# Kernel optimization log

Measured on AMD Instinct MI355X. Metric: run time of the kernel, lower is better.

## Reference

```python
import jax, jax.numpy as jnp
import numpy as np

N = 100000; E = 1600000; G = 512; L = 1000
FXD = 4; FXT = 5; H = 64; NOUT = 2

def setup_inputs() -> dict:
    key = jax.random.key(0)
    ks = jax.random.split(key, 16)
    x = jax.random.normal(ks[0], (N, FXD), dtype=jnp.float32)
    edge_index = jax.random.randint(ks[1], (2, E), 0, N, dtype=jnp.int64)
    # contiguous, non-empty graph assignment (sorted)
    batch = jnp.minimum(jnp.arange(N, dtype=jnp.int64) // (N // G), G - 1)
    target = jax.random.normal(ks[2], (G, L, FXT), dtype=jnp.float32)
    def lin(k, fi, fo):
        s = 1.0 / np.sqrt(fi)
        k1, k2 = jax.random.split(k)
        return (jax.random.uniform(k1, (fi, fo), jnp.float32, -s, s),
                jax.random.uniform(k2, (fo,), jnp.float32, -s, s))
    W1, b1 = lin(ks[3], FXD, H)
    W2, b2 = lin(ks[4], H, 2 * H)
    Wg, bg = lin(ks[5], 2 * H, H)
    s = 1.0 / np.sqrt(FXT * 3)
    Wc = jax.random.uniform(ks[6], (H, FXT, 3), jnp.float32, -s, s)  # OIH
    bc = jax.random.uniform(ks[7], (H,), jnp.float32, -s, s)
    Wt, bt = lin(ks[8], H, H)
    Wf, bf = lin(ks[9], 2 * H, H)
    Wo, bo = lin(ks[10], H, NOUT)
    return dict(x=x, edge_index=edge_index, batch=batch, target=target,
                W1=W1, b1=b1, W2=W2, b2=b2, Wg=Wg, bg=bg,
                Wc=Wc, bc=bc, Wt=Wt, bt=bt, Wf=Wf, bf=bf, Wo=Wo, bo=bo)

def _gcn_prep(edge_index):
    # add self-loops, compute symmetric normalization (PyG gcn_norm)
    loops = jnp.arange(N, dtype=edge_index.dtype)
    row = jnp.concatenate([edge_index[0], loops])
    col = jnp.concatenate([edge_index[1], loops])
    deg = jax.ops.segment_sum(jnp.ones_like(col, dtype=jnp.float32), col, num_segments=N)
    dis = jnp.where(deg > 0, jax.lax.rsqrt(deg), 0.0)
    norm = dis[row] * dis[col]  # [E+N]
    return row, col, norm

def _gcn_conv(h, row, col, norm):
    # gather-scale-scatter aggregation
    msg = h[row] * norm[:, None]
    return jax.ops.segment_sum(msg, col, num_segments=N)

def reference(x, edge_index, batch, target, W1, b1, W2, b2, Wg, bg, Wc, bc, Wt, bt, Wf, bf, Wo, bo):
    row, col, norm = _gcn_prep(edge_index)
    h = jax.nn.relu(_gcn_conv(x @ W1, row, col, norm) + b1)
    h = jax.nn.relu(_gcn_conv(h @ W2, row, col, norm) + b2)
    g = jax.ops.segment_max(h, batch, num_segments=G)  # global_max_pool [G, 2H]
    g = g @ Wg + bg  # dropout = identity (eval)
    t = jnp.transpose(target, (0, 2, 1))  # [G, FXT, L]
    t = jax.lax.conv_general_dilated(t, Wc, (1,), 'VALID',
                                     dimension_numbers=('NCH', 'OIH', 'NCH')) + bc[None, :, None]
    t = jax.nn.relu(t)
    t = jnp.max(t, axis=-1)  # AdaptiveMaxPool1d(1) [G, H]
    t = t @ Wt + bt
    xc = jnp.concatenate([g, t], axis=1)
    xc = jax.nn.relu(xc @ Wf + bf)
    return xc @ Wo + bo
```

## Files before the change

### kernel.cpp

```cpp
#include <hip/hip_runtime.h>
#include <hip/hip_bf16.h>

constexpr int N   = 100000;
constexpr int E   = 1600000;
constexpr int G   = 512;
constexpr int L   = 1000;
constexpr int NPG = 195;

constexpr int SLOTS = 48;
constexpr int NR2   = 256;
constexpr int RS2   = 391;
constexpr int PCAP2 = 6912;
constexpr int BCH   = 4096;

typedef __attribute__((ext_vector_type(8))) short bf16x8;
typedef __attribute__((ext_vector_type(4))) float f32x4;

__device__ __forceinline__ float bf2f(__hip_bfloat16 b) { return __bfloat162float(b); }
__device__ __forceinline__ float lo_bf(unsigned v) { return __uint_as_float(v << 16); }
__device__ __forceinline__ float hi_bf(unsigned v) { return __uint_as_float(v & 0xFFFF0000u); }
__device__ __forceinline__ unsigned packbf2(float a, float b) {
    __hip_bfloat16 ha = __float2bfloat16(a), hb = __float2bfloat16(b);
    unsigned short ua = *(unsigned short*)&ha, ub = *(unsigned short*)&hb;
    return (unsigned)ua | ((unsigned)ub << 16);
}


__global__ void k_init(int* __restrict__ pcnt, const float* __restrict__ W2,
                       short* __restrict__ W2hi, short* __restrict__ W2lo) {
    int i = blockIdx.x * 256 + threadIdx.x;
    if (i < NR2) pcnt[i] = 0;
    if (i < 64 * 128) {
        float w = W2[i];
        __hip_bfloat16 h = __float2bfloat16(w);
        float r = w - __bfloat162float(h);
        __hip_bfloat16 l = __float2bfloat16(r);
        W2hi[i] = *(short*)&h;
        W2lo[i] = *(short*)&l;
    }
}


__global__ void __launch_bounds__(256) k_part(
        const int* __restrict__ row, const int* __restrict__ col,
        int* __restrict__ pcnt, unsigned* __restrict__ precs) {
    __shared__ unsigned rec_s[BCH];
    __shared__ unsigned char rr_s[BCH];
    __shared__ int cnt_s[NR2], base_s[NR2], cur_s[NR2];
    int tid = threadIdx.x;
    cnt_s[tid] = 0;
    __syncthreads();
    int e0 = blockIdx.x * BCH;
    int nE = min(BCH, E - e0);
    for (int i = tid; i < nE; i += 256) {
        int c = __builtin_nontemporal_load(col + e0 + i);
        int r = __builtin_nontemporal_load(row + e0 + i);
        int rr = c / RS2;
        rec_s[i] = ((unsigned)r << 9) | (unsigned)(c - rr * RS2);
        rr_s[i] = (unsigned char)rr;
        atomicAdd(&cnt_s[rr], 1);
    }
    __syncthreads();
    base_s[tid] = atomicAdd(&pcnt[tid], cnt_s[tid]);
    cur_s[tid] = 0;
    __syncthreads();
    for (int i = tid; i < nE; i += 256) {
        int rr = rr_s[i];
        int p = base_s[rr] + atomicAdd(&cur_s[rr], 1);
        if (p < PCAP2) precs[rr * PCAP2 + p] = rec_s[i];
    }
}


__global__ void __launch_bounds__(256) k_sort(
        const int* __restrict__ pcnt, const unsigned* __restrict__ precs,
        int* __restrict__ slots, int* __restrict__ cursor, float* __restrict__ dis) {
    __shared__ unsigned recs[PCAP2];
    __shared__ int hist[512], off[512], off2[512], ps[256];
    int tid = threadIdx.x;
    int rr = blockIdx.x;
    int cnt = min(pcnt[rr], PCAP2);
    hist[tid] = 0; hist[tid + 256] = 0;
    __syncthreads();
    const unsigned* pr = precs + rr * PCAP2;
    for (int i = tid; i < cnt; i += 256) {
        unsigned r = pr[i];
        recs[i] = r;
        atomicAdd(&hist[r & 511], 1);
    }
    __syncthreads();
    int h0 = hist[2 * tid], h1 = hist[2 * tid + 1];
    int s = h0 + h1;
    ps[tid] = s;
    __syncthreads();
    for (int d = 1; d < 256; d <<= 1) {
        int v = (tid >= d) ? ps[tid - d] : 0;
        __syncthreads();
        ps[tid] += v;
        __syncthreads();
    }
    int excl = ps[tid] - s;
    off[2 * tid] = excl;       off[2 * tid + 1] = excl + h0;
    off2[2 * tid] = excl;      off2[2 * tid + 1] = excl + h0;
    __syncthreads();
    for (int ln = tid; ln < RS2; ln += 256) {
        int n = rr * RS2 + ln;
        if (n < N) {
            int c = hist[ln];
            dis[n] = rsqrtf((float)c + 1.0f);
            cursor[n] = n * SLOTS + min(c, SLOTS);
        }
    }
    for (int i = tid; i < cnt; i += 256) {
        unsigned r = recs[i];
        int ln = (int)(r & 511u);
        int p = atomicAdd(&off2[ln], 1);
        int j = p - off[ln];
        if (j < SLOTS) slots[(rr * RS2 + ln) * SLOTS + j] = (int)(r >> 9);
    }
}


__global__ void __launch_bounds__(256) k_gather_x(
        const int* __restrict__ cursor, const int* __restrict__ slots,
        const float* __restrict__ dis, const float4* __restrict__ x,
        float4* __restrict__ aggx) {
    int n = blockIdx.x * 256 + threadIdx.x;
    if (n >= N) return;
    int s = n * SLOTS;
    int cnt = cursor[n] - s;
    float dn = dis[n];
    float4 a = make_float4(0.f, 0.f, 0.f, 0.f);
    int j = 0;
    for (; j + 4 <= cnt; j += 4) {
        int s0 = slots[s + j], s1 = slots[s + j + 1],
            s2 = slots[s + j + 2], s3 = slots[s + j + 3];
        float w0 = dis[s0], w1 = dis[s1], w2 = dis[s2], w3 = dis[s3];
        float4 v0 = x[s0], v1 = x[s1], v2 = x[s2], v3 = x[s3];
        a.x = fmaf(v0.x, w0, a.x); a.y = fmaf(v0.y, w0, a.y);
        a.z = fmaf(v0.z, w0, a.z); a.w = fmaf(v0.w, w0, a.w);
        a.x = fmaf(v1.x, w1, a.x); a.y = fmaf(v1.y, w1, a.y);
        a.z = fmaf(v1.z, w1, a.z); a.w = fmaf(v1.w, w1, a.w);
        a.x = fmaf(v2.x, w2, a.x); a.y = fmaf(v2.y, w2, a.y);
        a.z = fmaf(v2.z, w2, a.z); a.w = fmaf(v2.w, w2, a.w);
        a.x = fmaf(v3.x, w3, a.x); a.y = fmaf(v3.y, w3, a.y);
        a.z = fmaf(v3.z, w3, a.z); a.w = fmaf(v3.w, w3, a.w);
    }
    for (; j < cnt; j++) {
        int sx = slots[s + j];
        float w = dis[sx];
        float4 v = x[sx];
        a.x = fmaf(v.x, w, a.x); a.y = fmaf(v.y, w, a.y);
        a.z = fmaf(v.z, w, a.z); a.w = fmaf(v.w, w, a.w);
    }
    float4 xs = x[n];
    float sl = dn * dn;
    a.x = fmaf(xs.x, sl, a.x * dn);
    a.y = fmaf(xs.y, sl, a.y * dn);
    a.z = fmaf(xs.z, sl, a.z * dn);
    a.w = fmaf(xs.w, sl, a.w * dn);
    aggx[n] = a;
}

__global__ void __launch_bounds__(256) k_layer1(
        const float4* __restrict__ aggx,
        const float* __restrict__ W1, const float* __restrict__ b1,
        __hip_bfloat16* __restrict__ h) {
    __shared__ float w1s[256];
    __shared__ float b1s[64];
    int tid = threadIdx.x;
    w1s[tid] = W1[tid];
    if (tid < 64) b1s[tid] = b1[tid];
    __syncthreads();
    int idx = blockIdx.x * 256 + tid;
    int n = idx >> 6;
    int f = idx & 63;
    if (n >= N) return;
    float4 a = aggx[n];
    float v = b1s[f];
    v = fmaf(a.x, w1s[f], v);
    v = fmaf(a.y, w1s[64 + f], v);
    v = fmaf(a.z, w1s[128 + f], v);
    v = fmaf(a.w, w1s[192 + f], v);
    h[idx] = __float2bfloat16(fmaxf(v, 0.0f));
}


__global__ void __launch_bounds__(256) k_gather_h(
        const int* __restrict__ cursor, const int* __restrict__ slots,
        const float* __restrict__ dis, const unsigned* __restrict__ h32,
        unsigned* __restrict__ aggh32) {
    __shared__ int   ls[8][SLOTS];
    __shared__ float lw[8][SLOTS];
    __shared__ int   lcnt[8];
    int tid = threadIdx.x;
    int nb = blockIdx.x * 8;
    if (tid < 8) {
        int node = nb + tid;
        lcnt[tid] = (node < N) ? (cursor[node] - node * SLOTS) : 0;
    }
    __syncthreads();
    for (int i = tid; i < 8 * SLOTS; i += 256) {
        int lo = i / SLOTS, j = i % SLOTS;
        if (j < lcnt[lo]) {
            int src = slots[(nb + lo) * SLOTS + j];
            ls[lo][j] = src;
            lw[lo][j] = dis[src];
        }
    }
    __syncthreads();
    int wid = tid >> 6, lane = tid & 63;
    int half = lane >> 5, li = lane & 31;
    int local = wid * 2 + half;
    int n = nb + local;
    if (n >= N) return;
    int cnt = lcnt[local];
    float dn = dis[n];
    float acc0 = 0.0f, acc1 = 0.0f;
    int j = 0;
    for (; j + 8 <= cnt; j += 8) {
        unsigned v[8]; float w[8];
        #pragma unroll
        for (int k = 0; k < 8; k++) {
            int src = ls[local][j + k];
            v[k] = h32[(size_t)src * 32 + li];
            w[k] = lw[local][j + k];
        }
        #pragma unroll
        for (int k = 0; k < 8; k++) {
            acc0 = fmaf(w[k], lo_bf(v[k]), acc0);
            acc1 = fmaf(w[k], hi_bf(v[k]), acc1);
        }
    }
    for (; j < cnt; j++) {
        int src = ls[local][j];
        unsigned v = h32[(size_t)src * 32 + li];
        float w = lw[local][j];
        acc0 = fmaf(w, lo_bf(v), acc0);
        acc1 = fmaf(w, hi_bf(v), acc1);
    }
    unsigned sv = h32[(size_t)n * 32 + li];
    acc0 = fmaf(dn, lo_bf(sv), acc0) * dn;
    acc1 = fmaf(dn, hi_bf(sv), acc1) * dn;
    aggh32[(size_t)n * 32 + li] = packbf2(acc0, acc1);
}


__global__ void __launch_bounds__(256) k_mfma_pool(
        const __hip_bfloat16* __restrict__ aggh,
        const short* __restrict__ W2hi, const short* __restrict__ W2lo,
        const float* __restrict__ b2, float* __restrict__ gbuf) {
    int tid = threadIdx.x;
    int wid = tid >> 6, lane = tid & 63;
    int m = lane & 15, quad = lane >> 4;
    int gi = blockIdx.x;
    int n0 = gi * NPG;
    int n1 = (gi == G - 1) ? N : n0 + NPG;
    int cb0 = wid * 32, cb1 = cb0 + 16;
    bf16x8 bh[2][2], bl[2][2];
    #pragma unroll
    for (int t = 0; t < 2; t++) {
        int cb = cb0 + t * 16;
        #pragma unroll
        for (int ks = 0; ks < 2; ks++) {
            bf16x8 hh, ll;
            #pragma unroll
            for (int j = 0; j < 8; j++) {
                int k = ks * 32 + quad * 8 + j;
                hh[j] = W2hi[k * 128 + cb + m];
                ll[j] = W2lo[k * 128 + cb + m];
            }
            bh[t][ks] = hh; bl[t][ks] = ll;
        }
    }
    float bias0 = b2[cb0 + m], bias1 = b2[cb1 + m];
    const short* ah = (const short*)aggh;
    float mx0 = 0.0f, mx1 = 0.0f;
    bf16x8 a0, a1;
    {
        const short* p = ah + (size_t)(n0 + m) * 64 + quad * 8;
        a0 = *(const bf16x8*)p;
        a1 = *(const bf16x8*)(p + 32);
    }
    for (int bn = n0; bn < n1; bn += 16) {
        bf16x8 na0 = a0, na1 = a1;
        if (bn + 16 < n1) {
            const short* p = ah + (size_t)(bn + 16 + m) * 64 + quad * 8;
            na0 = *(const bf16x8*)p;
            na1 = *(const bf16x8*)(p + 32);
        }
        f32x4 acc0 = {0.f, 0.f, 0.f, 0.f};
        f32x4 acc1 = {0.f, 0.f, 0.f, 0.f};
        acc0 = __builtin_amdgcn_mfma_f32_16x16x32_bf16(a0, bh[0][0], acc0, 0, 0, 0);
        acc0 = __builtin_amdgcn_mfma_f32_16x16x32_bf16(a1, bh[0][1], acc0, 0, 0, 0);
        acc0 = __builtin_amdgcn_mfma_f32_16x16x32_bf16(a0, bl[0][0], acc0, 0, 0, 0);
        acc0 = __builtin_amdgcn_mfma_f32_16x16x32_bf16(a1, bl[0][1], acc0, 0, 0, 0);
        acc1 = __builtin_amdgcn_mfma_f32_16x16x32_bf16(a0, bh[1][0], acc1, 0, 0, 0);
        acc1 = __builtin_amdgcn_mfma_f32_16x16x32_bf16(a1, bh[1][1], acc1, 0, 0, 0);
        acc1 = __builtin_amdgcn_mfma_f32_16x16x32_bf16(a0, bl[1][0], acc1, 0, 0, 0);
        acc1 = __builtin_amdgcn_mfma_f32_16x16x32_bf16(a1, bl[1][1], acc1, 0, 0, 0);
        int rb = bn + quad * 4;
        #pragma unroll
        for (int r = 0; r < 4; r++) {
            float v0 = fmaxf(acc0[r] + bias0, 0.0f);
            float v1 = fmaxf(acc1[r] + bias1, 0.0f);
            if (rb + r < n1) {
                mx0 = fmaxf(mx0, v0);
                mx1 = fmaxf(mx1, v1);
            }
        }
        a0 = na0; a1 = na1;
    }
    mx0 = fmaxf(mx0, __shfl_xor(mx0, 16));
    mx0 = fmaxf(mx0, __shfl_xor(mx0, 32));
    mx1 = fmaxf(mx1, __shfl_xor(mx1, 16));
    mx1 = fmaxf(mx1, __shfl_xor(mx1, 32));
    if (quad == 0) {
        gbuf[gi * 128 + cb0 + m] = mx0;
        gbuf[gi * 128 + cb1 + m] = mx1;
    }
}


__global__ void __launch_bounds__(256) k_conv(
        const float* __restrict__ target, const float* __restrict__ Wc,
        const float* __restrict__ bc, float* __restrict__ tb) {
    __shared__ float tg[L * 5];
    __shared__ float pm[4 * 64];
    int tid = threadIdx.x;
    int gi = blockIdx.x;
    const float* tsrc = target + (size_t)gi * (L * 5);
    for (int i = tid; i < L * 5; i += 256) tg[i] = tsrc[i];
    __syncthreads();
    int co = tid & 63, rr = tid >> 6;
    float wc[15];
    #pragma unroll
    for (int j = 0; j < 15; j++) wc[j] = Wc[co * 15 + j];
    int p0 = rr * 250;
    int pend = min(p0 + 250, 998);
    float a0 = tg[p0 * 5 + 0], a1 = tg[p0 * 5 + 1], a2 = tg[p0 * 5 + 2],
          a3 = tg[p0 * 5 + 3], a4 = tg[p0 * 5 + 4];
    float b0 = tg[p0 * 5 + 5], b1 = tg[p0 * 5 + 6], b2 = tg[p0 * 5 + 7],
          b3 = tg[p0 * 5 + 8], b4 = tg[p0 * 5 + 9];
    float m = -1e30f;
    for (int p = p0; p < pend; p++) {
        const float* cp = &tg[(p + 2) * 5];
        float c0 = cp[0], c1 = cp[1], c2 = cp[2], c3 = cp[3], c4 = cp[4];
        float v = 0.0f;
        v = fmaf(a0, wc[0],  v); v = fmaf(b0, wc[1],  v); v = fmaf(c0, wc[2],  v);
        v = fmaf(a1, wc[3],  v); v = fmaf(b1, wc[4],  v); v = fmaf(c1, wc[5],  v);
        v = fmaf(a2, wc[6],  v); v = fmaf(b2, wc[7],  v); v = fmaf(c2, wc[8],  v);
        v = fmaf(a3, wc[9],  v); v = fmaf(b3, wc[10], v); v = fmaf(c3, wc[11], v);
        v = fmaf(a4, wc[12], v); v = fmaf(b4, wc[13], v); v = fmaf(c4, wc[14], v);
        m = fmaxf(m, v);
        a0 = b0; a1 = b1; a2 = b2; a3 = b3; a4 = b4;
        b0 = c0; b1 = c1; b2 = c2; b3 = c3; b4 = c4;
    }
    pm[rr * 64 + co] = m;
    __syncthreads();
    if (tid < 64) {
        float mm = fmaxf(fmaxf(pm[tid], pm[64 + tid]), fmaxf(pm[128 + tid], pm[192 + tid]));
        tb[gi * 64 + tid] = fmaxf(mm + bc[tid], 0.0f);
    }
}


__global__ void __launch_bounds__(64) k_head(
        const float* __restrict__ gbuf, const float* __restrict__ tb,
        const float* __restrict__ Wg, const float* __restrict__ bg,
        const float* __restrict__ Wt, const float* __restrict__ bt,
        const float* __restrict__ Wf, const float* __restrict__ bf,
        const float* __restrict__ Wo, const float* __restrict__ bo,
        float* __restrict__ out) {
    __shared__ float grs[128], ts[64], g2s[64], t2s[64], xcs[64];
    int tid = threadIdx.x;
    int gi = blockIdx.x;
    grs[tid]      = gbuf[gi * 128 + tid];
    grs[64 + tid] = gbuf[gi * 128 + 64 + tid];
    ts[tid]       = tb[gi * 64 + tid];
    __syncthreads();
    float a = bg[tid];
    #pragma unroll 8
    for (int k = 0; k < 128; k++) a = fmaf(grs[k], Wg[k * 64 + tid], a);
    float b = bt[tid];
    #pragma unroll 8
    for (int k = 0; k < 64; k++) b = fmaf(ts[k], Wt[k * 64 + tid], b);
    g2s[tid] = a;
    t2s[tid] = b;
    __syncthreads();
    float c = bf[tid];
    #pragma unroll 8
    for (int k = 0; k < 64; k++) c = fmaf(g2s[k], Wf[k * 64 + tid], c);
    #pragma unroll 8
    for (int k = 0; k < 64; k++) c = fmaf(t2s[k], Wf[(64 + k) * 64 + tid], c);
    c = fmaxf(c, 0.0f);
    xcs[tid] = c;
    __syncthreads();
    if (tid < 2) {
        float o = bo[tid];
        for (int k = 0; k < 64; k++) o = fmaf(xcs[k], Wo[k * 2 + tid], o);
        out[gi * 2 + tid] = o;
    }
}


extern "C" void kernel_launch(void* const* d_in, const int* in_sizes, int n_in,
                              void* d_out, int out_size, void* d_ws, size_t ws_size,
                              hipStream_t stream) {
    const float* x      = (const float*)d_in[0];
    const int*   ei     = (const int*)d_in[1];
    const float* target = (const float*)d_in[3];
    const float* W1 = (const float*)d_in[4];
    const float* b1 = (const float*)d_in[5];
    const float* W2 = (const float*)d_in[6];
    const float* b2 = (const float*)d_in[7];
    const float* Wg = (const float*)d_in[8];
    const float* bg = (const float*)d_in[9];
    const float* Wc = (const float*)d_in[10];
    const float* bc = (const float*)d_in[11];
    const float* Wt = (const float*)d_in[12];
    const float* bt = (const float*)d_in[13];
    const float* Wf = (const float*)d_in[14];
    const float* bf = (const float*)d_in[15];
    const float* Wo = (const float*)d_in[16];
    const float* bo = (const float*)d_in[17];
    float* out = (float*)d_out;

    const int* row = ei;
    const int* col = ei + E;

    char* base = (char*)d_ws;
    size_t o = 0;
    auto alloc = [&](size_t bytes) -> void* {
        void* p = base + o;
        o = (o + bytes + 255) & ~(size_t)255;
        return p;
    };
    int*      cursor = (int*)     alloc((size_t)N * 4);
    float*    dis    = (float*)   alloc((size_t)N * 4);
    int*      slots  = (int*)     alloc((size_t)N * SLOTS * 4);
    int*      pcnt   = (int*)     alloc(NR2 * 4);
    unsigned* precs  = (unsigned*)alloc((size_t)NR2 * PCAP2 * 4);
    float*    aggx   = (float*)   alloc((size_t)N * 4 * 4);
    __hip_bfloat16* h    = (__hip_bfloat16*)alloc((size_t)N * 64 * 2);
    __hip_bfloat16* aggh = (__hip_bfloat16*)alloc((size_t)N * 64 * 2);
    short*    W2hi   = (short*)   alloc((size_t)64 * 128 * 2);
    short*    W2lo   = (short*)   alloc((size_t)64 * 128 * 2);
    float*    gbuf   = (float*)   alloc((size_t)G * 128 * 4);
    float*    tb     = (float*)   alloc((size_t)G * 64 * 4);

    k_init     <<<32, 256, 0, stream>>>(pcnt, W2, W2hi, W2lo);
    k_part     <<<(E + BCH - 1) / BCH, 256, 0, stream>>>(row, col, pcnt, precs);
    k_sort     <<<NR2, 256, 0, stream>>>(pcnt, precs, slots, cursor, dis);
    k_gather_x <<<(N + 255) / 256, 256, 0, stream>>>(cursor, slots, dis,
                                                     (const float4*)x, (float4*)aggx);
    k_layer1   <<<(N * 64 + 255) / 256, 256, 0, stream>>>((const float4*)aggx, W1, b1, h);
    k_gather_h <<<(N + 7) / 8, 256, 0, stream>>>(cursor, slots, dis,
                                                 (const unsigned*)h, (unsigned*)aggh);
    k_mfma_pool<<<G, 256, 0, stream>>>(aggh, W2hi, W2lo, b2, gbuf);
    k_conv     <<<G, 256, 0, stream>>>(target, Wc, bc, tb);
    k_head     <<<G, 64, 0, stream>>>(gbuf, tb, Wg, bg, Wt, bt, Wf, bf, Wo, bo, out);
}
```

Measured before the change: 278.0 us.

## Fuse layer-1 gather with linear layer and fold head MLP into pool kernel

Merges the x-aggregation gather and the layer-1 linear+ReLU into one kernel, staging aggregated features in shared memory and writing packed bf16 pairs. This removes the aggx intermediate buffer and one launch. It also moves the head MLP into the tail of the MFMA pooling kernel, run by the first wavefront after a block sync, which drops gbuf and the separate head launch. The cost is that the head now runs serially in one wave per block, and conv must finish before pooling.

```diff
diff --git a/kernel.cpp b/kernel.cpp
--- a/kernel.cpp
+++ b/kernel.cpp
@@ -121,68 +121,75 @@
 }
 
 
-__global__ void __launch_bounds__(256) k_gather_x(
+__global__ void __launch_bounds__(256) k_gxl1(
         const int* __restrict__ cursor, const int* __restrict__ slots,
         const float* __restrict__ dis, const float4* __restrict__ x,
-        float4* __restrict__ aggx) {
-    int n = blockIdx.x * 256 + threadIdx.x;
-    if (n >= N) return;
-    int s = n * SLOTS;
-    int cnt = cursor[n] - s;
-    float dn = dis[n];
-    float4 a = make_float4(0.f, 0.f, 0.f, 0.f);
-    int j = 0;
-    for (; j + 4 <= cnt; j += 4) {
-        int s0 = slots[s + j], s1 = slots[s + j + 1],
-            s2 = slots[s + j + 2], s3 = slots[s + j + 3];
-        float w0 = dis[s0], w1 = dis[s1], w2 = dis[s2], w3 = dis[s3];
-        float4 v0 = x[s0], v1 = x[s1], v2 = x[s2], v3 = x[s3];
-        a.x = fmaf(v0.x, w0, a.x); a.y = fmaf(v0.y, w0, a.y);
-        a.z = fmaf(v0.z, w0, a.z); a.w = fmaf(v0.w, w0, a.w);
-        a.x = fmaf(v1.x, w1, a.x); a.y = fmaf(v1.y, w1, a.y);
-        a.z = fmaf(v1.z, w1, a.z); a.w = fmaf(v1.w, w1, a.w);
-        a.x = fmaf(v2.x, w2, a.x); a.y = fmaf(v2.y, w2, a.y);
-        a.z = fmaf(v2.z, w2, a.z); a.w = fmaf(v2.w, w2, a.w);
-        a.x = fmaf(v3.x, w3, a.x); a.y = fmaf(v3.y, w3, a.y);
-        a.z = fmaf(v3.z, w3, a.z); a.w = fmaf(v3.w, w3, a.w);
-    }
-    for (; j < cnt; j++) {
-        int sx = slots[s + j];
-        float w = dis[sx];
-        float4 v = x[sx];
-        a.x = fmaf(v.x, w, a.x); a.y = fmaf(v.y, w, a.y);
-        a.z = fmaf(v.z, w, a.z); a.w = fmaf(v.w, w, a.w);
-    }
-    float4 xs = x[n];
-    float sl = dn * dn;
-    a.x = fmaf(xs.x, sl, a.x * dn);
-    a.y = fmaf(xs.y, sl, a.y * dn);
-    a.z = fmaf(xs.z, sl, a.z * dn);
-    a.w = fmaf(xs.w, sl, a.w * dn);
-    aggx[n] = a;
-}
-
-__global__ void __launch_bounds__(256) k_layer1(
-        const float4* __restrict__ aggx,
         const float* __restrict__ W1, const float* __restrict__ b1,
-        __hip_bfloat16* __restrict__ h) {
+        unsigned* __restrict__ h32) {
+    __shared__ float ax[256][4];
     __shared__ float w1s[256];
     __shared__ float b1s[64];
     int tid = threadIdx.x;
     w1s[tid] = W1[tid];
     if (tid < 64) b1s[tid] = b1[tid];
-    __syncthreads();
-    int idx = blockIdx.x * 256 + tid;
-    int n = idx >> 6;
-    int f = idx & 63;
-    if (n >= N) return;
-    float4 a = aggx[n];
-    float v = b1s[f];
-    v = fmaf(a.x, w1s[f], v);
-    v = fmaf(a.y, w1s[64 + f], v);
-    v = fmaf(a.z, w1s[128 + f], v);
-    v = fmaf(a.w, w1s[192 + f], v);
-    h[idx] = __float2bfloat16(fmaxf(v, 0.0f));
+    int nb = blockIdx.x * 256;
+    int n = nb + tid;
+    float4 a = make_float4(0.f, 0.f, 0.f, 0.f);
+    if (n < N) {
+        int s = n * SLOTS;
+        int cnt = cursor[n] - s;
+        float dn = dis[n];
+        int j = 0;
+        for (; j + 4 <= cnt; j += 4) {
+            int s0 = slots[s + j], s1 = slots[s + j + 1],
+                s2 = slots[s + j + 2], s3 = slots[s + j + 3];
+            float w0 = dis[s0], w1 = dis[s1], w2 = dis[s2], w3 = dis[s3];
+            float4 v0 = x[s0], v1 = x[s1], v2 = x[s2], v3 = x[s3];
+            a.x = fmaf(v0.x, w0, a.x); a.y = fmaf(v0.y, w0, a.y);
+            a.z = fmaf(v0.z, w0, a.z); a.w = fmaf(v0.w, w0, a.w);
+            a.x = fmaf(v1.x, w1, a.x); a.y = fmaf(v1.y, w1, a.y);
+            a.z = fmaf(v1.z, w1, a.z); a.w = fmaf(v1.w, w1, a.w);
+            a.x = fmaf(v2.x, w2, a.x); a.y = fmaf(v2.y, w2, a.y);
+            a.z = fmaf(v2.z, w2, a.z); a.w = fmaf(v2.w, w2, a.w);
+            a.x = fmaf(v3.x, w3, a.x); a.y = fmaf(v3.y, w3, a.y);
+            a.z = fmaf(v3.z, w3, a.z); a.w = fmaf(v3.w, w3, a.w);
+        }
+        for (; j < cnt; j++) {
+            int sx = slots[s + j];
+            float w = dis[sx];
+            float4 v = x[sx];
+            a.x = fmaf(v.x, w, a.x); a.y = fmaf(v.y, w, a.y);
+            a.z = fmaf(v.z, w, a.z); a.w = fmaf(v.w, w, a.w);
+        }
+        float4 xs = x[n];
+        float sl = dn * dn;
+        a.x = fmaf(xs.x, sl, a.x * dn);
+        a.y = fmaf(xs.y, sl, a.y * dn);
+        a.z = fmaf(xs.z, sl, a.z * dn);
+        a.w = fmaf(xs.w, sl, a.w * dn);
+    }
+    ax[tid][0] = a.x; ax[tid][1] = a.y; ax[tid][2] = a.z; ax[tid][3] = a.w;
+    __syncthreads();
+    int p = tid & 31, r0 = tid >> 5;
+    int f0 = 2 * p, f1 = 2 * p + 1;
+    float wA0 = w1s[f0],       wB0 = w1s[f1];
+    float wA1 = w1s[64 + f0],  wB1 = w1s[64 + f1];
+    float wA2 = w1s[128 + f0], wB2 = w1s[128 + f1];
+    float wA3 = w1s[192 + f0], wB3 = w1s[192 + f1];
+    float bb0 = b1s[f0], bb1 = b1s[f1];
+    #pragma unroll 4
+    for (int i = 0; i < 32; i++) {
+        int ln = r0 + 8 * i;
+        int node = nb + ln;
+        if (node >= N) break;
+        float v0 = bb0, v1 = bb1;
+        float g0 = ax[ln][0], g1 = ax[ln][1], g2 = ax[ln][2], g3 = ax[ln][3];
+        v0 = fmaf(g0, wA0, v0); v1 = fmaf(g0, wB0, v1);
+        v0 = fmaf(g1, wA1, v0); v1 = fmaf(g1, wB1, v1);
+        v0 = fmaf(g2, wA2, v0); v1 = fmaf(g2, wB2, v1);
+        v0 = fmaf(g3, wA3, v0); v1 = fmaf(g3, wB3, v1);
+        h32[(size_t)node * 32 + p] = packbf2(fmaxf(v0, 0.0f), fmaxf(v1, 0.0f));
+    }
 }
 
 
@@ -243,82 +250,6 @@
     acc0 = fmaf(dn, lo_bf(sv), acc0) * dn;
     acc1 = fmaf(dn, hi_bf(sv), acc1) * dn;
     aggh32[(size_t)n * 32 + li] = packbf2(acc0, acc1);
-}
-
-
-__global__ void __launch_bounds__(256) k_mfma_pool(
-        const __hip_bfloat16* __restrict__ aggh,
-        const short* __restrict__ W2hi, const short* __restrict__ W2lo,
-        const float* __restrict__ b2, float* __restrict__ gbuf) {
-    int tid = threadIdx.x;
-    int wid = tid >> 6, lane = tid & 63;
-    int m = lane & 15, quad = lane >> 4;
-    int gi = blockIdx.x;
-    int n0 = gi * NPG;
-    int n1 = (gi == G - 1) ? N : n0 + NPG;
-    int cb0 = wid * 32, cb1 = cb0 + 16;
-    bf16x8 bh[2][2], bl[2][2];
-    #pragma unroll
-    for (int t = 0; t < 2; t++) {
-        int cb = cb0 + t * 16;
-        #pragma unroll
-        for (int ks = 0; ks < 2; ks++) {
-            bf16x8 hh, ll;
-            #pragma unroll
-            for (int j = 0; j < 8; j++) {
-                int k = ks * 32 + quad * 8 + j;
-                hh[j] = W2hi[k * 128 + cb + m];
-                ll[j] = W2lo[k * 128 + cb + m];
-            }
-            bh[t][ks] = hh; bl[t][ks] = ll;
-        }
-    }
-    float bias0 = b2[cb0 + m], bias1 = b2[cb1 + m];
-    const short* ah = (const short*)aggh;
-    float mx0 = 0.0f, mx1 = 0.0f;
-    bf16x8 a0, a1;
-    {
-        const short* p = ah + (size_t)(n0 + m) * 64 + quad * 8;
-        a0 = *(const bf16x8*)p;
-        a1 = *(const bf16x8*)(p + 32);
-    }
-    for (int bn = n0; bn < n1; bn += 16) {
-        bf16x8 na0 = a0, na1 = a1;
-        if (bn + 16 < n1) {
-            const short* p = ah + (size_t)(bn + 16 + m) * 64 + quad * 8;
-            na0 = *(const bf16x8*)p;
-            na1 = *(const bf16x8*)(p + 32);
-        }
-        f32x4 acc0 = {0.f, 0.f, 0.f, 0.f};
-        f32x4 acc1 = {0.f, 0.f, 0.f, 0.f};
-        acc0 = __builtin_amdgcn_mfma_f32_16x16x32_bf16(a0, bh[0][0], acc0, 0, 0, 0);
-        acc0 = __builtin_amdgcn_mfma_f32_16x16x32_bf16(a1, bh[0][1], acc0, 0, 0, 0);
-        acc0 = __builtin_amdgcn_mfma_f32_16x16x32_bf16(a0, bl[0][0], acc0, 0, 0, 0);
-        acc0 = __builtin_amdgcn_mfma_f32_16x16x32_bf16(a1, bl[0][1], acc0, 0, 0, 0);
-        acc1 = __builtin_amdgcn_mfma_f32_16x16x32_bf16(a0, bh[1][0], acc1, 0, 0, 0);
-        acc1 = __builtin_amdgcn_mfma_f32_16x16x32_bf16(a1, bh[1][1], acc1, 0, 0, 0);
-        acc1 = __builtin_amdgcn_mfma_f32_16x16x32_bf16(a0, bl[1][0], acc1, 0, 0, 0);
-        acc1 = __builtin_amdgcn_mfma_f32_16x16x32_bf16(a1, bl[1][1], acc1, 0, 0, 0);
-        int rb = bn + quad * 4;
-        #pragma unroll
-        for (int r = 0; r < 4; r++) {
-            float v0 = fmaxf(acc0[r] + bias0, 0.0f);
-            float v1 = fmaxf(acc1[r] + bias1, 0.0f);
-            if (rb + r < n1) {
-                mx0 = fmaxf(mx0, v0);
-                mx1 = fmaxf(mx1, v1);
-            }
-        }
-        a0 = na0; a1 = na1;
-    }
-    mx0 = fmaxf(mx0, __shfl_xor(mx0, 16));
-    mx0 = fmaxf(mx0, __shfl_xor(mx0, 32));
-    mx1 = fmaxf(mx1, __shfl_xor(mx1, 16));
-    mx1 = fmaxf(mx1, __shfl_xor(mx1, 32));
-    if (quad == 0) {
-        gbuf[gi * 128 + cb0 + m] = mx0;
-        gbuf[gi * 128 + cb1 + m] = mx1;
-    }
 }
 
 
@@ -365,41 +296,107 @@
 }
 
 
-__global__ void __launch_bounds__(64) k_head(
-        const float* __restrict__ gbuf, const float* __restrict__ tb,
+__global__ void __launch_bounds__(256) k_mfma_pool(
+        const __hip_bfloat16* __restrict__ aggh,
+        const short* __restrict__ W2hi, const short* __restrict__ W2lo,
+        const float* __restrict__ b2, const float* __restrict__ tb,
         const float* __restrict__ Wg, const float* __restrict__ bg,
         const float* __restrict__ Wt, const float* __restrict__ bt,
         const float* __restrict__ Wf, const float* __restrict__ bf,
         const float* __restrict__ Wo, const float* __restrict__ bo,
         float* __restrict__ out) {
-    __shared__ float grs[128], ts[64], g2s[64], t2s[64], xcs[64];
-    int tid = threadIdx.x;
+    __shared__ float gvec[128], ts[64], g2s[64], t2s[64], xcs[64];
+    int tid = threadIdx.x;
+    int wid = tid >> 6, lane = tid & 63;
+    int m = lane & 15, quad = lane >> 4;
     int gi = blockIdx.x;
-    grs[tid]      = gbuf[gi * 128 + tid];
-    grs[64 + tid] = gbuf[gi * 128 + 64 + tid];
-    ts[tid]       = tb[gi * 64 + tid];
-    __syncthreads();
-    float a = bg[tid];
-    #pragma unroll 8
-    for (int k = 0; k < 128; k++) a = fmaf(grs[k], Wg[k * 64 + tid], a);
-    float b = bt[tid];
-    #pragma unroll 8
-    for (int k = 0; k < 64; k++) b = fmaf(ts[k], Wt[k * 64 + tid], b);
-    g2s[tid] = a;
-    t2s[tid] = b;
-    __syncthreads();
-    float c = bf[tid];
-    #pragma unroll 8
-    for (int k = 0; k < 64; k++) c = fmaf(g2s[k], Wf[k * 64 + tid], c);
-    #pragma unroll 8
-    for (int k = 0; k < 64; k++) c = fmaf(t2s[k], Wf[(64 + k) * 64 + tid], c);
-    c = fmaxf(c, 0.0f);
-    xcs[tid] = c;
-    __syncthreads();
-    if (tid < 2) {
-        float o = bo[tid];
-        for (int k = 0; k < 64; k++) o = fmaf(xcs[k], Wo[k * 2 + tid], o);
-        out[gi * 2 + tid] = o;
+    int n0 = gi * NPG;
+    int n1 = (gi == G - 1) ? N : n0 + NPG;
+    int cb0 = wid * 32, cb1 = cb0 + 16;
+    bf16x8 bh[2][2], bl[2][2];
+    #pragma unroll
+    for (int t = 0; t < 2; t++) {
+        int cb = cb0 + t * 16;
+        #pragma unroll
+        for (int ks = 0; ks < 2; ks++) {
+            bf16x8 hh, ll;
+            #pragma unroll
+            for (int j = 0; j < 8; j++) {
+                int k = ks * 32 + quad * 8 + j;
+                hh[j] = W2hi[k * 128 + cb + m];
+                ll[j] = W2lo[k * 128 + cb + m];
+            }
+            bh[t][ks] = hh; bl[t][ks] = ll;
+        }
+    }
+    float bias0 = b2[cb0 + m], bias1 = b2[cb1 + m];
+    const short* ah = (const short*)aggh;
+    float mx0 = 0.0f, mx1 = 0.0f;
+    bf16x8 a0, a1;
+    {
+        const short* p = ah + (size_t)(n0 + m) * 64 + quad * 8;
+        a0 = *(const bf16x8*)p;
+        a1 = *(const bf16x8*)(p + 32);
+    }
+    for (int bn = n0; bn < n1; bn += 16) {
+        bf16x8 na0 = a0, na1 = a1;
+        if (bn + 16 < n1) {
+            const short* p = ah + (size_t)(bn + 16 + m) * 64 + quad * 8;
+            na0 = *(const bf16x8*)p;
+            na1 = *(const bf16x8*)(p + 32);
+        }
+        f32x4 acc0 = {0.f, 0.f, 0.f, 0.f};
+        f32x4 acc1 = {0.f, 0.f, 0.f, 0.f};
+        acc0 = __builtin_amdgcn_mfma_f32_16x16x32_bf16(a0, bh[0][0], acc0, 0, 0, 0);
+        acc0 = __builtin_amdgcn_mfma_f32_16x16x32_bf16(a1, bh[0][1], acc0, 0, 0, 0);
+        acc0 = __builtin_amdgcn_mfma_f32_16x16x32_bf16(a0, bl[0][0], acc0, 0, 0, 0);
+        acc0 = __builtin_amdgcn_mfma_f32_16x16x32_bf16(a1, bl[0][1], acc0, 0, 0, 0);
+        acc1 = __builtin_amdgcn_mfma_f32_16x16x32_bf16(a0, bh[1][0], acc1, 0, 0, 0);
+        acc1 = __builtin_amdgcn_mfma_f32_16x16x32_bf16(a1, bh[1][1], acc1, 0, 0, 0);
+        acc1 = __builtin_amdgcn_mfma_f32_16x16x32_bf16(a0, bl[1][0], acc1, 0, 0, 0);
+        acc1 = __builtin_amdgcn_mfma_f32_16x16x32_bf16(a1, bl[1][1], acc1, 0, 0, 0);
+        int rb = bn + quad * 4;
+        #pragma unroll
+        for (int r = 0; r < 4; r++) {
+            float v0 = fmaxf(acc0[r] + bias0, 0.0f);
+            float v1 = fmaxf(acc1[r] + bias1, 0.0f);
+            if (rb + r < n1) {
+                mx0 = fmaxf(mx0, v0);
+                mx1 = fmaxf(mx1, v1);
+            }
+        }
+        a0 = na0; a1 = na1;
+    }
+    mx0 = fmaxf(mx0, __shfl_xor(mx0, 16));
+    mx0 = fmaxf(mx0, __shfl_xor(mx0, 32));
+    mx1 = fmaxf(mx1, __shfl_xor(mx1, 16));
+    mx1 = fmaxf(mx1, __shfl_xor(mx1, 32));
+    if (quad == 0) {
+        gvec[cb0 + m] = mx0;
+        gvec[cb1 + m] = mx1;
+    }
+    __syncthreads();
+    if (wid == 0) {
+        ts[lane] = tb[gi * 64 + lane];
+        float a = bg[lane];
+        #pragma unroll 8
+        for (int k = 0; k < 128; k++) a = fmaf(gvec[k], Wg[k * 64 + lane], a);
+        float b = bt[lane];
+        #pragma unroll 8
+        for (int k = 0; k < 64; k++) b = fmaf(ts[k], Wt[k * 64 + lane], b);
+        g2s[lane] = a;
+        t2s[lane] = b;
+        float c = bf[lane];
+        #pragma unroll 8
+        for (int k = 0; k < 64; k++) c = fmaf(g2s[k], Wf[k * 64 + lane], c);
+        #pragma unroll 8
+        for (int k = 0; k < 64; k++) c = fmaf(t2s[k], Wf[(64 + k) * 64 + lane], c);
+        xcs[lane] = fmaxf(c, 0.0f);
+        if (lane < 2) {
+            float o = bo[lane];
+            for (int k = 0; k < 64; k++) o = fmaf(xcs[k], Wo[k * 2 + lane], o);
+            out[gi * 2 + lane] = o;
+        }
     }
 }
 
@@ -441,23 +438,22 @@
     int*      slots  = (int*)     alloc((size_t)N * SLOTS * 4);
     int*      pcnt   = (int*)     alloc(NR2 * 4);
     unsigned* precs  = (unsigned*)alloc((size_t)NR2 * PCAP2 * 4);
-    float*    aggx   = (float*)   alloc((size_t)N * 4 * 4);
     __hip_bfloat16* h    = (__hip_bfloat16*)alloc((size_t)N * 64 * 2);
     __hip_bfloat16* aggh = (__hip_bfloat16*)alloc((size_t)N * 64 * 2);
     short*    W2hi   = (short*)   alloc((size_t)64 * 128 * 2);
     short*    W2lo   = (short*)   alloc((size_t)64 * 128 * 2);
-    float*    gbuf   = (float*)   alloc((size_t)G * 128 * 4);
     float*    tb     = (float*)   alloc((size_t)G * 64 * 4);
+    (void)    alloc(4096);
 
     k_init     <<<32, 256, 0, stream>>>(pcnt, W2, W2hi, W2lo);
     k_part     <<<(E + BCH - 1) / BCH, 256, 0, stream>>>(row, col, pcnt, precs);
     k_sort     <<<NR2, 256, 0, stream>>>(pcnt, precs, slots, cursor, dis);
-    k_gather_x <<<(N + 255) / 256, 256, 0, stream>>>(cursor, slots, dis,
-                                                     (const float4*)x, (float4*)aggx);
-    k_layer1   <<<(N * 64 + 255) / 256, 256, 0, stream>>>((const float4*)aggx, W1, b1, h);
+    k_gxl1     <<<(N + 255) / 256, 256, 0, stream>>>(cursor, slots, dis,
+                                                     (const float4*)x, W1, b1,
+                                                     (unsigned*)h);
     k_gather_h <<<(N + 7) / 8, 256, 0, stream>>>(cursor, slots, dis,
                                                  (const unsigned*)h, (unsigned*)aggh);
-    k_mfma_pool<<<G, 256, 0, stream>>>(aggh, W2hi, W2lo, b2, gbuf);
     k_conv     <<<G, 256, 0, stream>>>(target, Wc, bc, tb);
-    k_head     <<<G, 64, 0, stream>>>(gbuf, tb, Wg, bg, Wt, bt, Wf, bf, Wo, bo, out);
-}
+    k_mfma_pool<<<G, 256, 0, stream>>>(aggh, W2hi, W2lo, b2, tb, Wg, bg, Wt, bt,
+                                       Wf, bf, Wo, bo, out);
+}
```

After: 261.5 us. 1.06x faster.
